# Performance work log

Measured on AMD Instinct MI355X. Metric: run time of the kernel, lower is better.

Reference implementation:

```python
import jax, jax.numpy as jnp
import numpy as np

N_NODES = 100000
N_EDGES = 1600000
IN_FEATS = 256
NUM_HEADS = 4
OUT_FEATS = 64
NEG_SLOPE = 0.2


def setup_inputs() -> dict:
    key = jax.random.key(0)
    k1, k2, k3, k4, k5, k6 = jax.random.split(key, 6)
    feat = jax.random.normal(k1, (N_NODES, IN_FEATS), dtype=jnp.float32)
    # VarianceScaling(scale=sqrt(2), fan_avg) ~ std = sqrt(2*sqrt(2)/(fan_in+fan_out))
    w_std = float(np.sqrt(np.sqrt(2.0) * 2.0 / (IN_FEATS + NUM_HEADS * OUT_FEATS)))
    W = jax.random.normal(k2, (IN_FEATS, NUM_HEADS * OUT_FEATS), dtype=jnp.float32) * w_std
    a_std = float(np.sqrt(np.sqrt(2.0) * 2.0 / (1 + OUT_FEATS)))
    attn_l = jax.random.normal(k3, (1, NUM_HEADS, OUT_FEATS), dtype=jnp.float32) * a_std
    attn_r = jax.random.normal(k4, (1, NUM_HEADS, OUT_FEATS), dtype=jnp.float32) * a_std
    src = jax.random.randint(k5, (N_EDGES,), 0, N_NODES, dtype=jnp.int32)
    dst = jax.random.randint(k6, (N_EDGES,), 0, N_NODES, dtype=jnp.int32)
    return {"feat": feat, "W": W, "attn_l": attn_l, "attn_r": attn_r, "src": src, "dst": dst}


def reference(feat, W, attn_l, attn_r, src, dst):
    N = feat.shape[0]
    H, D = attn_l.shape[1], attn_l.shape[2]
    # projection: [N, H, D]
    ft = jnp.reshape(feat @ W, (N, H, D))
    # per-node attention logits: [N, H]
    el = jnp.sum(ft * attn_l, axis=-1)
    er = jnp.sum(ft * attn_r, axis=-1)
    # per-edge logits (u_add_v) + LeakyReLU: [E, H]
    e = jax.nn.leaky_relu(el[src] + er[dst], negative_slope=NEG_SLOPE)
    # segmented softmax over incoming edges of each destination node
    seg_max = jax.ops.segment_max(e, dst, num_segments=N)  # [N, H]
    seg_max = jnp.where(jnp.isfinite(seg_max), seg_max, 0.0)
    ex = jnp.exp(e - seg_max[dst])  # [E, H]
    seg_sum = jax.ops.segment_sum(ex, dst, num_segments=N)  # [N, H]
    a = ex / seg_sum[dst]  # [E, H]
    # weighted scatter-sum aggregation (u_mul_e then sum): [N, H, D]
    msgs = ft[src] * a[:, :, None]  # [E, H, D]
    rst = jax.ops.segment_sum(msgs, dst, num_segments=N)
    return rst
```

## Files before the change

### kernel.cpp

```cpp
#include <hip/hip_runtime.h>

#define HEADS 4
#define DH 64
#define NHID 256
#define KIN 256
#define NEG_SLOPE 0.2f
#define CAP 128

typedef __attribute__((ext_vector_type(8))) short short8;
typedef __attribute__((ext_vector_type(4))) float f32x4;

__device__ inline float bf2f(unsigned short u) {
  union { unsigned int i; float f; } v; v.i = ((unsigned int)u) << 16; return v.f;
}
__device__ inline unsigned short f2bf(float f) {
  union { float f; unsigned int i; } v; v.f = f;
  unsigned int r = v.i + 0x7FFF + ((v.i >> 16) & 1);
  return (unsigned short)(r >> 16);
}

__global__ void k_cvtW(const float* __restrict__ W, unsigned short* __restrict__ Wt) {
  int n = blockIdx.x, k = threadIdx.x;
  Wt[n * 256 + k] = f2bf(W[k * 256 + n]);
}

__global__ __launch_bounds__(256, 2) void k_gemm(
    const float* __restrict__ feat, const unsigned short* __restrict__ Wt,
    const float* __restrict__ al, const float* __restrict__ ar,
    unsigned short* __restrict__ ftb, float* __restrict__ el,
    float* __restrict__ er, int M)
{
  __shared__ unsigned short As[64 * 32];
  __shared__ unsigned short Bs[256 * 32];
  const int t = threadIdx.x;
  const int lane = t & 63;
  const int w = t >> 6;
  const int row0 = blockIdx.x * 64;

  f32x4 acc[4][4] = {};

  const int ra = t >> 2, ca = t & 3;
  const int arow = min(row0 + ra, M - 1);
  const int adst = ra * 64 + ((ca ^ ((ra >> 1) & 3)) * 16);

  for (int k0 = 0; k0 < KIN; k0 += 32) {
    const float* ga = feat + (size_t)arow * KIN + k0 + ca * 8;
    float4 v0 = *(const float4*)ga;
    float4 v1 = *(const float4*)(ga + 4);
    short8 pk;
    pk[0] = (short)f2bf(v0.x); pk[1] = (short)f2bf(v0.y);
    pk[2] = (short)f2bf(v0.z); pk[3] = (short)f2bf(v0.w);
    pk[4] = (short)f2bf(v1.x); pk[5] = (short)f2bf(v1.y);
    pk[6] = (short)f2bf(v1.z); pk[7] = (short)f2bf(v1.w);
    *(short8*)((char*)As + adst) = pk;
    #pragma unroll
    for (int j = 0; j < 4; ++j) {
      int n = j * 64 + (t >> 2);
      int c = t & 3;
      const unsigned short* gb = Wt + n * 256 + k0 + ((c ^ ((n >> 1) & 3)) * 8);
      __builtin_amdgcn_global_load_lds(
          (const __attribute__((address_space(1))) void*)gb,
          (__attribute__((address_space(3))) void*)((char*)Bs + j * 4096 + t * 16),
          16, 0, 0);
    }
    __syncthreads();
    const int i = lane & 15, kc = lane >> 4;
    short8 af[4], bf[4];
    #pragma unroll
    for (int m = 0; m < 4; ++m) {
      int r = m * 16 + i;
      af[m] = *(const short8*)((const char*)As + r * 64 + ((kc ^ ((r >> 1) & 3)) * 16));
    }
    #pragma unroll
    for (int n = 0; n < 4; ++n) {
      int nr = w * 64 + n * 16 + i;
      bf[n] = *(const short8*)((const char*)Bs + nr * 64 + ((kc ^ ((nr >> 1) & 3)) * 16));
    }
    #pragma unroll
    for (int m = 0; m < 4; ++m)
      #pragma unroll
      for (int n = 0; n < 4; ++n)
        acc[m][n] = __builtin_amdgcn_mfma_f32_16x16x32_bf16(af[m], bf[n], acc[m][n], 0, 0, 0);
    __syncthreads();
  }

  const int ci = lane & 15, rg = lane >> 4;
  #pragma unroll
  for (int m = 0; m < 4; ++m) {
    #pragma unroll
    for (int r = 0; r < 4; ++r) {
      int grow = row0 + m * 16 + rg * 4 + r;
      if (grow < M) {
        unsigned short* fp = ftb + (size_t)grow * NHID + w * 64;
        #pragma unroll
        for (int n = 0; n < 4; ++n) fp[n * 16 + ci] = f2bf(acc[m][n][r]);
      }
    }
  }
  float alv[4], arv[4];
  #pragma unroll
  for (int n = 0; n < 4; ++n) {
    alv[n] = al[w * DH + n * 16 + ci];
    arv[n] = ar[w * DH + n * 16 + ci];
  }
  #pragma unroll
  for (int m = 0; m < 4; ++m) {
    #pragma unroll
    for (int r = 0; r < 4; ++r) {
      float pl = 0.f, pr = 0.f;
      #pragma unroll
      for (int n = 0; n < 4; ++n) {
        pl += acc[m][n][r] * alv[n];
        pr += acc[m][n][r] * arv[n];
      }
      pl += __shfl_xor(pl, 1); pl += __shfl_xor(pl, 2);
      pl += __shfl_xor(pl, 4); pl += __shfl_xor(pl, 8);
      pr += __shfl_xor(pr, 1); pr += __shfl_xor(pr, 2);
      pr += __shfl_xor(pr, 4); pr += __shfl_xor(pr, 8);
      if (ci == 0) {
        int grow = row0 + m * 16 + rg * 4 + r;
        if (grow < M) { el[grow * HEADS + w] = pl; er[grow * HEADS + w] = pr; }
      }
    }
  }
}

__global__ void k_fill(const int* __restrict__ src, const int* __restrict__ dst,
                       int* __restrict__ deg, int* __restrict__ bucket, int E) {
  int e = blockIdx.x * 256 + threadIdx.x;
  if (e < E) {
    int d = dst[e];
    int p = atomicAdd(&deg[d], 1);
    bucket[(size_t)d * CAP + p] = src[e];
  }
}

__global__ __launch_bounds__(256) void k_aggr(
    const unsigned short* __restrict__ ftb, const float* __restrict__ el,
    const float* __restrict__ er, const int* __restrict__ deg,
    const int* __restrict__ bucket, float* __restrict__ out, int N)
{
  int n = blockIdx.x * 4 + (threadIdx.x >> 6);
  int lane = threadIdx.x & 63;
  if (n >= N) return;
  int q  = lane >> 4;
  int ql = lane & 15;
  int hh = ql >> 2;
  int start = n * CAP;
  int end = start + deg[n];
  const short8* ft8 = (const short8*)ftb;
  float acc[16] = {};
  float ws = 0.f;
  if (end > start) {
    float erh = er[n * HEADS + hh];
    int last = end - 1;
    int eA = start + q;
    int eB = eA + 4;
    int sB = bucket[min(eB, last)];
    {
      int sA = bucket[min(eA, last)];
      float lxA = el[sA * 4 + hh];
      short8 fa0 = ft8[(size_t)sA * 32 + ql * 2];
      short8 fa1 = ft8[(size_t)sA * 32 + ql * 2 + 1];
      for (int e0 = start; e0 < end; e0 += 4) {
        int sC = bucket[min(e0 + 8 + q, last)];
        float lxB = el[sB * 4 + hh];
        short8 fb0 = ft8[(size_t)sB * 32 + ql * 2];
        short8 fb1 = ft8[(size_t)sB * 32 + ql * 2 + 1];
        bool v = (e0 + q) < end;
        float x = lxA + erh;
        x = x > 0.f ? x : NEG_SLOPE * x;
        float ex = v ? __expf(x) : 0.f;
        ws += ex;
        #pragma unroll
        for (int j = 0; j < 8; ++j) acc[j]     += ex * bf2f((unsigned short)fa0[j]);
        #pragma unroll
        for (int j = 0; j < 8; ++j) acc[j + 8] += ex * bf2f((unsigned short)fa1[j]);
        sB = sC; lxA = lxB; fa0 = fb0; fa1 = fb1;
      }
    }
  }
  ws += __shfl_xor(ws, 16); ws += __shfl_xor(ws, 32);
  #pragma unroll
  for (int j = 0; j < 16; ++j) {
    acc[j] += __shfl_xor(acc[j], 16);
    acc[j] += __shfl_xor(acc[j], 32);
  }
  if (q == 0) {
    float inv = (end > start) ? 1.f / ws : 0.f;
    float* op = out + (size_t)n * NHID + ql * 16;
    #pragma unroll
    for (int j4 = 0; j4 < 4; ++j4)
      *(float4*)(op + j4 * 4) = make_float4(acc[j4 * 4] * inv, acc[j4 * 4 + 1] * inv,
                                            acc[j4 * 4 + 2] * inv, acc[j4 * 4 + 3] * inv);
  }
}

extern "C" void kernel_launch(void* const* d_in, const int* in_sizes, int n_in,
                              void* d_out, int out_size, void* d_ws, size_t ws_size,
                              hipStream_t stream)
{
  const float* feat = (const float*)d_in[0];
  const float* W    = (const float*)d_in[1];
  const float* al   = (const float*)d_in[2];
  const float* ar   = (const float*)d_in[3];
  const int*   src  = (const int*)d_in[4];
  const int*   dst  = (const int*)d_in[5];
  const int M = in_sizes[0] / KIN;
  const int E = in_sizes[4];
  float* out = (float*)d_out;

  char* base = (char*)d_ws;
  size_t off = 0;
  auto alloc = [&](size_t b) { char* p = base + off; off = (off + b + 255) & ~(size_t)255; return p; };
  unsigned short* ftb = (unsigned short*)alloc((size_t)M * NHID * sizeof(unsigned short));
  unsigned short* Wt  = (unsigned short*)alloc(256 * 256 * sizeof(unsigned short));
  float* el     = (float*)alloc((size_t)M * HEADS * sizeof(float));
  float* er     = (float*)alloc((size_t)M * HEADS * sizeof(float));
  int*   deg    = (int*)alloc((size_t)M * sizeof(int));
  int*   bucket = (int*)alloc((size_t)M * CAP * sizeof(int));
  (void)ws_size; (void)n_in; (void)out_size;

  hipMemsetAsync(deg, 0, (size_t)M * sizeof(int), stream);

  k_cvtW<<<256, 256, 0, stream>>>(W, Wt);
  k_fill<<<(E + 255) / 256, 256, 0, stream>>>(src, dst, deg, bucket, E);
  k_gemm<<<(M + 63) / 64, 256, 0, stream>>>(feat, Wt, al, ar, ftb, el, er, M);
  k_aggr<<<(M + 3) / 4, 256, 0, stream>>>(ftb, el, er, deg, bucket, out, M);
}
```

Measured before the change: 306.4 us.

## Preload full A tile into LDS and double-buffer W tiles in GEMM

```diff
diff --git a/kernel.cpp b/kernel.cpp
--- a/kernel.cpp
+++ b/kernel.cpp
@@ -30,8 +30,8 @@
     unsigned short* __restrict__ ftb, float* __restrict__ el,
     float* __restrict__ er, int M)
 {
-  __shared__ unsigned short As[64 * 32];
-  __shared__ unsigned short Bs[256 * 32];
+  __shared__ unsigned short As[64 * 256];
+  __shared__ unsigned short Bs[2][256 * 32];
   const int t = threadIdx.x;
   const int lane = t & 63;
   const int w = t >> 6;
@@ -39,42 +39,64 @@
 
   f32x4 acc[4][4] = {};
 
-  const int ra = t >> 2, ca = t & 3;
-  const int arow = min(row0 + ra, M - 1);
-  const int adst = ra * 64 + ((ca ^ ((ra >> 1) & 3)) * 16);
-
-  for (int k0 = 0; k0 < KIN; k0 += 32) {
-    const float* ga = feat + (size_t)arow * KIN + k0 + ca * 8;
-    float4 v0 = *(const float4*)ga;
-    float4 v1 = *(const float4*)(ga + 4);
+  float4 av0[8], av1[8];
+  #pragma unroll
+  for (int j = 0; j < 8; ++j) {
+    int g = j * 256 + t;
+    int r = g >> 5, c = g & 31;
+    const float* ga = feat + (size_t)min(row0 + r, M - 1) * KIN + c * 8;
+    av0[j] = *(const float4*)ga;
+    av1[j] = *(const float4*)(ga + 4);
+  }
+  const int bn0 = t >> 2, bkc = t & 3;
+  #pragma unroll
+  for (int j = 0; j < 4; ++j) {
+    int n = j * 64 + bn0;
+    const unsigned short* gb = Wt + n * 256 + ((bkc ^ ((n >> 1) & 3)) * 8);
+    __builtin_amdgcn_global_load_lds(
+        (const __attribute__((address_space(1))) void*)gb,
+        (__attribute__((address_space(3))) void*)((char*)Bs[0] + j * 4096 + t * 16),
+        16, 0, 0);
+  }
+  #pragma unroll
+  for (int j = 0; j < 8; ++j) {
+    int g = j * 256 + t;
+    int r = g >> 5, c = g & 31;
     short8 pk;
-    pk[0] = (short)f2bf(v0.x); pk[1] = (short)f2bf(v0.y);
-    pk[2] = (short)f2bf(v0.z); pk[3] = (short)f2bf(v0.w);
-    pk[4] = (short)f2bf(v1.x); pk[5] = (short)f2bf(v1.y);
-    pk[6] = (short)f2bf(v1.z); pk[7] = (short)f2bf(v1.w);
-    *(short8*)((char*)As + adst) = pk;
-    #pragma unroll
-    for (int j = 0; j < 4; ++j) {
-      int n = j * 64 + (t >> 2);
-      int c = t & 3;
-      const unsigned short* gb = Wt + n * 256 + k0 + ((c ^ ((n >> 1) & 3)) * 8);
-      __builtin_amdgcn_global_load_lds(
-          (const __attribute__((address_space(1))) void*)gb,
-          (__attribute__((address_space(3))) void*)((char*)Bs + j * 4096 + t * 16),
-          16, 0, 0);
-    }
-    __syncthreads();
-    const int i = lane & 15, kc = lane >> 4;
+    pk[0] = (short)f2bf(av0[j].x); pk[1] = (short)f2bf(av0[j].y);
+    pk[2] = (short)f2bf(av0[j].z); pk[3] = (short)f2bf(av0[j].w);
+    pk[4] = (short)f2bf(av1[j].x); pk[5] = (short)f2bf(av1[j].y);
+    pk[6] = (short)f2bf(av1[j].z); pk[7] = (short)f2bf(av1[j].w);
+    *(short8*)((char*)As + r * 512 + ((c ^ (r & 7)) * 16)) = pk;
+  }
+  __syncthreads();
+
+  const int i = lane & 15, kc = lane >> 4;
+  for (int kt = 0; kt < 8; ++kt) {
+    if (kt < 7) {
+      int k0 = (kt + 1) * 32;
+      #pragma unroll
+      for (int j = 0; j < 4; ++j) {
+        int n = j * 64 + bn0;
+        const unsigned short* gb = Wt + n * 256 + k0 + ((bkc ^ ((n >> 1) & 3)) * 8);
+        __builtin_amdgcn_global_load_lds(
+            (const __attribute__((address_space(1))) void*)gb,
+            (__attribute__((address_space(3))) void*)((char*)Bs[(kt + 1) & 1] + j * 4096 + t * 16),
+            16, 0, 0);
+      }
+    }
     short8 af[4], bf[4];
     #pragma unroll
     for (int m = 0; m < 4; ++m) {
       int r = m * 16 + i;
-      af[m] = *(const short8*)((const char*)As + r * 64 + ((kc ^ ((r >> 1) & 3)) * 16));
-    }
+      int c = kt * 4 + kc;
+      af[m] = *(const short8*)((const char*)As + r * 512 + ((c ^ (r & 7)) * 16));
+    }
+    const char* bbase = (const char*)Bs[kt & 1];
     #pragma unroll
     for (int n = 0; n < 4; ++n) {
       int nr = w * 64 + n * 16 + i;
-      bf[n] = *(const short8*)((const char*)Bs + nr * 64 + ((kc ^ ((nr >> 1) & 3)) * 16));
+      bf[n] = *(const short8*)(bbase + nr * 64 + ((kc ^ ((nr >> 1) & 3)) * 16));
     }
     #pragma unroll
     for (int m = 0; m < 4; ++m)
```

After: 291.2 us. 1.05x faster.
